# Performance work log

Measured on AMD Instinct MI355X. Metric: run time of the kernel, lower is better.

## Reference

```python
import jax, jax.numpy as jnp
import numpy as np

B, S, E, A = 64, 1024, 512, 128


def setup_inputs() -> dict:
    key = jax.random.key(0)
    ks = jax.random.split(key, 12)
    sc = 0.02
    states = jax.random.normal(ks[0], (B, S, E), jnp.float32)
    cls_token = jax.random.normal(ks[1], (B, E), jnp.float32)
    # ragged lengths in [2, S]; force at least one full-length row so padded width == S-1
    lengths = jax.random.randint(ks[2], (B,), 2, S + 1).at[0].set(S).astype(jnp.int32)
    position_action = (jax.random.randint(ks[3], (B,), 0, S) % (lengths - 1)).astype(jnp.int32)
    symbol_action = jax.random.randint(ks[4], (B,), 0, A).astype(jnp.int32)
    W1p = jax.random.normal(ks[5], (2 * E, 2 * E), jnp.float32) * sc
    b1p = jnp.zeros((2 * E,), jnp.float32)
    w2p = jax.random.normal(ks[6], (2 * E,), jnp.float32) * sc
    b2p = jnp.zeros((1,), jnp.float32)
    W1s = jax.random.normal(ks[7], (2 * E, 2 * E), jnp.float32) * sc
    b1s = jnp.zeros((2 * E,), jnp.float32)
    W2s = jax.random.normal(ks[8], (2 * E, A), jnp.float32) * sc
    b2s = jnp.zeros((A,), jnp.float32)
    Wc1 = jax.random.normal(ks[9], (E, E), jnp.float32) * sc
    bc1 = jnp.zeros((E,), jnp.float32)
    wc2 = jax.random.normal(ks[10], (E,), jnp.float32) * sc
    bc2 = jnp.zeros((1,), jnp.float32)
    return dict(states=states, cls_token=cls_token, W1p=W1p, b1p=b1p, w2p=w2p, b2p=b2p,
                W1s=W1s, b1s=b1s, W2s=W2s, b2s=b2s, Wc1=Wc1, bc1=bc1, wc2=wc2, bc2=bc2,
                lengths=lengths, position_action=position_action, symbol_action=symbol_action)


def reference(states, cls_token, W1p, b1p, w2p, b2p, W1s, b1s, W2s, b2s,
              Wc1, bc1, wc2, bc2, lengths, position_action, symbol_action):
    b, s, e = states.shape
    # --- get_adjacent_pairs + position_actor MLP, fused (no [.,2E] concat materialized) ---
    first, second = states[:, :-1], states[:, 1:]            # (B, S-1, E) each
    h = jax.nn.relu(jnp.einsum('bse,ef->bsf', first, W1p[:e])
                    + jnp.einsum('bse,ef->bsf', second, W1p[e:]) + b1p)  # (B, S-1, 2E)
    scores = jnp.einsum('bsf,f->bs', h, w2p) + b2p            # (B, S-1)
    # --- map_scores_to_sentences: pad invalid pair slots with -inf ---
    pos_mask = jnp.arange(s - 1)[None, :] < (lengths - 1)[:, None]
    scores = jnp.where(pos_mask, scores, -jnp.inf)
    logp = jax.nn.log_softmax(scores, axis=1)
    logp_pos = jnp.take_along_axis(logp, position_action[:, None], axis=1)[:, 0]
    logp_m = jnp.where(pos_mask, logp, 0.0)                   # safe for -inf slots
    ent_pos = -jnp.sum(jnp.exp(logp) * logp_m, axis=1)
    # --- symbol head on the pair embedding at the chosen split position ---
    bidx = jnp.arange(b)
    e1 = states[bidx, position_action]                        # (B, E)
    e2 = states[bidx, position_action + 1]                    # (B, E)
    sh = jax.nn.relu(e1 @ W1s[:e] + e2 @ W1s[e:] + b1s)       # (B, 2E)
    slogp = jax.nn.log_softmax(sh @ W2s + b2s, axis=1)        # (B, A)
    logp_sym = jnp.take_along_axis(slogp, symbol_action[:, None], axis=1)[:, 0]
    ent_sym = -jnp.sum(jnp.exp(slogp) * slogp, axis=1)
    # --- critic on cls token ---
    val = jax.nn.relu(cls_token @ Wc1 + bc1) @ wc2 + bc2      # (B,)
    return jnp.stack([logp_pos, logp_sym, val, ent_pos, ent_sym], axis=0)  # (5, B)
```

## Files before the change

### kernel.cpp

```cpp
#include <hip/hip_runtime.h>
#include <stdint.h>

#define BDIM 64
#define SDIM 1024
#define EDIM 512
#define ADIM 128
#define KDIM 1024
#define NDIM 1024

typedef unsigned short u16;
typedef __attribute__((ext_vector_type(8))) short short8;
typedef __attribute__((ext_vector_type(4))) float floatx4;
typedef const __attribute__((address_space(1))) void as1_void;
typedef __attribute__((address_space(3))) void as3_void;

__device__ inline u16 f2bf(float f){
  unsigned int u = __float_as_uint(f);
  u += 0x7fffu + ((u >> 16) & 1u);
  return (u16)(u >> 16);
}

__global__ __launch_bounds__(1024) void k_prep(
    const float* __restrict__ states,
    const float* __restrict__ W1p, const int* __restrict__ lengths,
    const int* __restrict__ pos_action,
    u16* __restrict__ sbf, u16* __restrict__ wt,
    int* __restrict__ rows, int* __restrict__ aux,
    float* __restrict__ scores)
{
  __shared__ float smem[64*65];
  const int blk = blockIdx.x, tid = threadIdx.x;

  if (blk < 1024){
    int i = blk*1024 + tid;
#pragma unroll
    for (int it = 0; it < 4; ++it, i += 1048576){
      int row = i >> 6;
      int s = row & 1023, b = row >> 10;
      if (s < lengths[b]){
        const float4* sp = (const float4*)states + (size_t)i*2;
        float4 a = sp[0], c = sp[1];
        short8 v;
        v[0]=(short)f2bf(a.x); v[1]=(short)f2bf(a.y); v[2]=(short)f2bf(a.z); v[3]=(short)f2bf(a.w);
        v[4]=(short)f2bf(c.x); v[5]=(short)f2bf(c.y); v[6]=(short)f2bf(c.z); v[7]=(short)f2bf(c.w);
        ((short8*)sbf)[i] = v;
      }
    }
    return;
  }
  if (blk < 1280){
    float (*tile)[65] = (float(*)[65])smem;
    int tb = blk - 1024;
    int zi = tb*1024 + tid;
    if (zi < 65536) scores[zi] = 0.f;
    int k0 = (tb & 15)*64, n0 = (tb >> 4)*64;
    int tx = tid & 63, ty = tid >> 6;
    for (int j = ty; j < 64; j += 16) tile[j][tx] = W1p[(size_t)(k0+j)*NDIM + n0 + tx];
    __syncthreads();
    for (int j = ty; j < 64; j += 16) wt[(size_t)(n0+j)*KDIM + k0 + tx] = f2bf(tile[tx][j]);
    return;
  }
  {
    __shared__ int scum[65];
    if (tid == 0){
      int c = 0;
      for (int b = 0; b < 64; ++b){ scum[b] = c; c += lengths[b] - 1; }
      scum[64] = c;
    }
    __syncthreads();
    if (tid < 65) aux[tid] = scum[tid];
    if (tid == 0){
      aux[70] = scum[64];
      aux[71] = (scum[64] + 127) >> 7;
    }
    if (tid < 64) rows[65472 + tid] = (tid << 10) + pos_action[tid];
    for (int b = 0; b < 64; ++b){
      int base = scum[b], L = scum[b+1] - scum[b];
      for (int i2 = tid; i2 < L; i2 += 1024) rows[base + i2] = (b << 10) + i2;
    }
  }
}

__global__ __launch_bounds__(256, 2) void k_gemm_scores(
    const u16* __restrict__ sbf, const u16* __restrict__ wt,
    const float* __restrict__ b1p, const float* __restrict__ w2p,
    const int* __restrict__ rows, const int* __restrict__ aux,
    float* __restrict__ scores,
    const float* __restrict__ cls,
    const float* __restrict__ W1s, const float* __restrict__ b1s,
    const float* __restrict__ Wc1, const float* __restrict__ bc1,
    const float* __restrict__ wc2, const float* __restrict__ bc2,
    float* __restrict__ sh, float* __restrict__ out)
{
  __shared__ short8 LDS[2048];
  const int tid = threadIdx.x;
  const int j = blockIdx.x;

  if (j < 8){
    short8* Ash = LDS;
    short8* Bsh = LDS + 512;
    const int w = tid >> 6, l = tid & 63;
    const int n0 = j * 128;
    const int lrow8 = l >> 3;
    const int c = (l & 7) ^ lrow8;
    const char* sbase = (const char*)sbf;
    int offA[2];
#pragma unroll
    for (int i = 0; i < 2; ++i){
      int mloc = (w*2 + i)*8 + lrow8;
      int rs = rows[65472 + mloc];
      offA[i] = rs*1024 + c*16;
    }
    const int r = l & 15, q = l >> 4;
    const int wm = w & 1, wn = w >> 1;
    int aIdx[2], bIdx[4];
#pragma unroll
    for (int i = 0; i < 2; ++i){
      int m = wm*32 + i*16 + r;
      aIdx[i] = m*8 + (q ^ (r & 7));
    }
#pragma unroll
    for (int i = 0; i < 4; ++i){
      int n = wn*64 + i*16 + r;
      bIdx[i] = n*8 + (q ^ (r & 7));
    }
    const int kt8 = tid >> 5, nq = tid & 31;
    floatx4 acc[2][4];
#pragma unroll
    for (int a = 0; a < 2; ++a)
#pragma unroll
      for (int b = 0; b < 4; ++b) acc[a][b] = (floatx4)(0.0f);

    for (int step = 0; step < 16; ++step){
      __syncthreads();
#pragma unroll
      for (int i = 0; i < 2; ++i)
        __builtin_amdgcn_global_load_lds((as1_void*)(sbase + offA[i] + step*128),
                                         (as3_void*)((char*)Ash + (w*2 + i)*1024), 16, 0, 0);
      const float* wsrc = W1s + (size_t)(step*64 + kt8*8)*1024 + n0 + nq*4;
      float v[8][4];
#pragma unroll
      for (int kk = 0; kk < 8; ++kk)
        *(float4*)v[kk] = *(const float4*)(wsrc + (size_t)kk*1024);
#pragma unroll
      for (int jj = 0; jj < 4; ++jj){
        short8 c8;
#pragma unroll
        for (int kk = 0; kk < 8; ++kk) c8[kk] = (short)f2bf(v[kk][jj]);
        int R = nq*4 + jj;
        Bsh[R*8 + (kt8 ^ (R & 7))] = c8;
      }
      __syncthreads();
#pragma unroll
      for (int kh = 0; kh < 2; ++kh){
        short8 af[2], bf[4];
#pragma unroll
        for (int i = 0; i < 2; ++i) af[i] = Ash[aIdx[i] ^ (kh*4)];
#pragma unroll
        for (int i = 0; i < 4; ++i) bf[i] = Bsh[bIdx[i] ^ (kh*4)];
#pragma unroll
        for (int mi = 0; mi < 2; ++mi)
#pragma unroll
          for (int ni = 0; ni < 4; ++ni)
            acc[mi][ni] = __builtin_amdgcn_mfma_f32_16x16x32_bf16(af[mi], bf[ni], acc[mi][ni], 0, 0, 0);
      }
    }
#pragma unroll
    for (int mi = 0; mi < 2; ++mi)
#pragma unroll
      for (int ni = 0; ni < 4; ++ni){
        int row = wm*32 + mi*16 + q*4;
        int col = n0 + wn*64 + ni*16 + r;
        floatx4 a = acc[mi][ni];
        float bb = b1s[col];
#pragma unroll
        for (int jj = 0; jj < 4; ++jj)
          sh[(row + jj)*1024 + col] = fmaxf(a[jj] + bb, 0.f);
      }
    return;
  }
  if (j < 72){
    float* xs = (float*)LDS;
    float* r2 = (float*)LDS + 512;
    int b = j - 8;
    xs[tid]       = cls[b*EDIM + tid];
    xs[tid + 256] = cls[b*EDIM + tid + 256];
    __syncthreads();
    float a0 = 0.f, a1 = 0.f;
#pragma unroll 8
    for (int k = 0; k < 512; ++k){
      float x = xs[k];
      a0 = fmaf(x, Wc1[(size_t)k*EDIM + tid],       a0);
      a1 = fmaf(x, Wc1[(size_t)k*EDIM + tid + 256], a1);
    }
    float p = fmaxf(a0 + bc1[tid],       0.f) * wc2[tid]
            + fmaxf(a1 + bc1[tid + 256], 0.f) * wc2[tid + 256];
    for (int off = 32; off; off >>= 1) p += __shfl_xor(p, off);
    if ((tid & 63) == 0) r2[tid >> 6] = p;
    __syncthreads();
    if (tid == 0) out[128 + b] = bc2[0] + r2[0] + r2[1] + r2[2] + r2[3];
    return;
  }

  short8* Ash = LDS;
  short8* Bsh = LDS + 1024;
  const int w = tid >> 6, l = tid & 63;
  const int jg = j - 72;
  const int tl = ((jg >> 6) << 3) | (jg & 7);
  const int nt = (jg >> 3) & 7;
  const int total = aux[70];
  if (tl >= aux[71]) return;

  const int lrow8 = l >> 3;
  const int c = (l & 7) ^ lrow8;
  const char* sbase = (const char*)sbf;
  const char* wbase = (const char*)wt;
  int offA[4], offB[4];
#pragma unroll
  for (int i = 0; i < 4; ++i){
    int mloc = (w*4 + i)*8 + lrow8;
    int mg = tl*128 + mloc;
    if (mg >= total) mg = 0;
    int rs = rows[mg];
    offA[i] = rs*1024 + c*16;
    int nloc = (w*4 + i)*8 + lrow8;
    offB[i] = (nt*128 + nloc)*2048 + c*16;
  }

  const int r = l & 15, q = l >> 4;
  const int wm = w & 1, wn = w >> 1;
  int aIdx[4], bIdx[4];
#pragma unroll
  for (int i = 0; i < 4; ++i){
    int m = wm*64 + i*16 + r;
    aIdx[i] = m*8 + (q ^ (r & 7));
    int n = wn*64 + i*16 + r;
    bIdx[i] = n*8 + (q ^ (r & 7));
  }

  floatx4 acc[4][4];
#pragma unroll
  for (int a = 0; a < 4; ++a)
#pragma unroll
    for (int b = 0; b < 4; ++b) acc[a][b] = (floatx4)(0.0f);

  for (int step = 0; step < 16; ++step){
    const int ktb = step * 128;
    __syncthreads();
#pragma unroll
    for (int i = 0; i < 4; ++i){
      __builtin_amdgcn_global_load_lds((as1_void*)(sbase + offA[i] + ktb),
                                       (as3_void*)((char*)Ash + (w*4 + i)*1024), 16, 0, 0);
    }
#pragma unroll
    for (int i = 0; i < 4; ++i){
      __builtin_amdgcn_global_load_lds((as1_void*)(wbase + offB[i] + ktb),
                                       (as3_void*)((char*)Bsh + (w*4 + i)*1024), 16, 0, 0);
    }
    __syncthreads();
#pragma unroll
    for (int kh = 0; kh < 2; ++kh){
      short8 af[4], bf[4];
#pragma unroll
      for (int i = 0; i < 4; ++i) af[i] = Ash[aIdx[i] ^ (kh*4)];
#pragma unroll
      for (int i = 0; i < 4; ++i) bf[i] = Bsh[bIdx[i] ^ (kh*4)];
#pragma unroll
      for (int mi = 0; mi < 4; ++mi)
#pragma unroll
        for (int ni = 0; ni < 4; ++ni)
          acc[mi][ni] = __builtin_amdgcn_mfma_f32_16x16x32_bf16(af[mi], bf[ni], acc[mi][ni], 0, 0, 0);
    }
  }

  const int mrow0 = tl*128 + wm*64;
  const int ncol0 = nt*128 + wn*64;
#pragma unroll
  for (int mi = 0; mi < 4; ++mi){
    float t0 = 0.f, t1 = 0.f, t2 = 0.f, t3 = 0.f;
#pragma unroll
    for (int ni = 0; ni < 4; ++ni){
      int n = ncol0 + ni*16 + r;
      float bb = b1p[n], ww = w2p[n];
      floatx4 a = acc[mi][ni];
      t0 += fmaxf(a[0] + bb, 0.f) * ww;
      t1 += fmaxf(a[1] + bb, 0.f) * ww;
      t2 += fmaxf(a[2] + bb, 0.f) * ww;
      t3 += fmaxf(a[3] + bb, 0.f) * ww;
    }
#pragma unroll
    for (int off = 1; off < 16; off <<= 1){
      t0 += __shfl_xor(t0, off);
      t1 += __shfl_xor(t1, off);
      t2 += __shfl_xor(t2, off);
      t3 += __shfl_xor(t3, off);
    }
    if (r == 0){
      int row = mrow0 + mi*16 + q*4;
      if (row + 0 < total) atomicAdd(&scores[row + 0], t0);
      if (row + 1 < total) atomicAdd(&scores[row + 1], t1);
      if (row + 2 < total) atomicAdd(&scores[row + 2], t2);
      if (row + 3 < total) atomicAdd(&scores[row + 3], t3);
    }
  }
}

__global__ __launch_bounds__(1024) void k_post(
    const float* __restrict__ scores, const float* __restrict__ sh,
    const float* __restrict__ W2s, const float* __restrict__ b2s,
    const int* __restrict__ aux, const int* __restrict__ lengths,
    const int* __restrict__ pos_action, const int* __restrict__ sym_action,
    float* __restrict__ out)
{
  __shared__ float smem[2208];
  const int blk = blockIdx.x, tid = threadIdx.x;
  if (blk < 64){
    float* sc   = smem;
    float* red  = smem + 1024;
    float* red2 = smem + 1040;
    int b = blk;
    int L = lengths[b] - 1;
    const float* sp = scores + aux[b];
    float mx = -1e30f;
    for (int s = tid; s < L; s += 1024){
      float v = sp[s];
      sc[s] = v;
      mx = fmaxf(mx, v);
    }
    for (int off = 32; off; off >>= 1) mx = fmaxf(mx, __shfl_xor(mx, off));
    if ((tid & 63) == 0) red[tid >> 6] = mx;
    __syncthreads();
    mx = -1e30f;
#pragma unroll
    for (int jj = 0; jj < 16; ++jj) mx = fmaxf(mx, red[jj]);
    float se = 0.f, ses = 0.f;
    for (int s = tid; s < L; s += 1024){
      float v = sc[s];
      float e = expf(v - mx);
      se += e; ses += e * v;
    }
    for (int off = 32; off; off >>= 1){ se += __shfl_xor(se, off); ses += __shfl_xor(ses, off); }
    __syncthreads();
    if ((tid & 63) == 0){ red[tid >> 6] = se; red2[tid >> 6] = ses; }
    __syncthreads();
    if (tid == 0){
      float S = 0.f, SS = 0.f;
#pragma unroll
      for (int jj = 0; jj < 16; ++jj){ S += red[jj]; SS += red2[jj]; }
      float logZ = logf(S);
      int pa = pos_action[b];
      out[b]       = sc[pa] - mx - logZ;
      out[192 + b] = mx + logZ - SS / S;
    }
    return;
  }
  {
    float* xs  = smem;
    float* red = smem + 1024;
    float* lg  = smem + 2048;
    float* r2  = smem + 2176;
    float* r3  = smem + 2192;
    int b = blk - 64;
    xs[tid] = sh[b*1024 + tid];
    __syncthreads();
    int n = tid & 127;
    int f0 = (tid >> 7) * 128;
    float acc = 0.f;
#pragma unroll 8
    for (int jj = 0; jj < 128; ++jj){
      int f = f0 + jj;
      acc = fmaf(xs[f], W2s[(size_t)f*ADIM + n], acc);
    }
    red[tid] = acc;
    __syncthreads();
    if (tid < 128){
      float s = b2s[tid];
#pragma unroll
      for (int jj = 0; jj < 8; ++jj) s += red[tid + jj*128];
      lg[tid] = s;
    }
    __syncthreads();
    float v = (tid < 128) ? lg[tid] : -1e30f;
    float mx = v;
    for (int off = 32; off; off >>= 1) mx = fmaxf(mx, __shfl_xor(mx, off));
    if ((tid & 63) == 0) r2[tid >> 6] = mx;
    __syncthreads();
    mx = -1e30f;
#pragma unroll
    for (int jj = 0; jj < 16; ++jj) mx = fmaxf(mx, r2[jj]);
    float e = (tid < 128) ? expf(v - mx) : 0.f;
    float se = e, ses = (tid < 128) ? e * v : 0.f;
    for (int off = 32; off; off >>= 1){ se += __shfl_xor(se, off); ses += __shfl_xor(ses, off); }
    __syncthreads();
    if ((tid & 63) == 0){ r2[tid >> 6] = se; r3[tid >> 6] = ses; }
    __syncthreads();
    if (tid == 0){
      float S = 0.f, SS = 0.f;
#pragma unroll
      for (int jj = 0; jj < 16; ++jj){ S += r2[jj]; SS += r3[jj]; }
      float logZ = logf(S);
      out[64 + b]  = lg[sym_action[b]] - mx - logZ;
      out[256 + b] = mx + logZ - SS / S;
    }
  }
}

extern "C" void kernel_launch(void* const* d_in, const int* in_sizes, int n_in,
                              void* d_out, int out_size, void* d_ws, size_t ws_size,
                              hipStream_t stream){
  const float* states = (const float*)d_in[0];
  const float* cls    = (const float*)d_in[1];
  const float* W1p    = (const float*)d_in[2];
  const float* b1p    = (const float*)d_in[3];
  const float* w2p    = (const float*)d_in[4];
  const float* W1s    = (const float*)d_in[6];
  const float* b1s    = (const float*)d_in[7];
  const float* W2s    = (const float*)d_in[8];
  const float* b2s    = (const float*)d_in[9];
  const float* Wc1    = (const float*)d_in[10];
  const float* bc1    = (const float*)d_in[11];
  const float* wc2    = (const float*)d_in[12];
  const float* bc2    = (const float*)d_in[13];
  const int* lengths  = (const int*)d_in[14];
  const int* pos_a    = (const int*)d_in[15];
  const int* sym_a    = (const int*)d_in[16];
  float* out = (float*)d_out;

  char* ws = (char*)d_ws;
  u16* sbf      = (u16*)ws;
  u16* wt       = (u16*)(ws + 67108864);
  float* scores = (float*)(ws + 69206016);
  float* sh     = (float*)(ws + 69468160);
  int* rows     = (int*)(ws + 69730304);
  int* aux      = (int*)(ws + 69992448);

  k_prep<<<1281, 1024, 0, stream>>>(states, W1p, lengths, pos_a, sbf, wt, rows, aux, scores);
  k_gemm_scores<<<4168, 256, 0, stream>>>(sbf, wt, b1p, w2p, rows, aux, scores,
                                          cls, W1s, b1s, Wc1, bc1, wc2, bc2, sh, out);
  k_post<<<128, 1024, 0, stream>>>(scores, sh, W2s, b2s, aux, lengths, pos_a, sym_a, out);
}
```

Before: 303.7 us.

## Run critic MLP as bf16 MFMA tiles and parallelize row-index build

The critic head, previously computed as 64 scalar-FMA blocks (one per batch row), becomes 4 MFMA blocks over 128-column slices of Wc1. A bf16 copy of the cls token is prepared in the prep kernel, and partial value dot products are reduced with atomics into an output preinitialized with bc2. The row-index/prefix-sum construction, formerly done by one serial block, is split across 64 blocks, one per batch. This trims launch size and serial prep work, but adds bf16 rounding to the critic and atomic, order-dependent summation.

```diff
diff --git a/kernel.cpp b/kernel.cpp
--- a/kernel.cpp
+++ b/kernel.cpp
@@ -21,12 +21,12 @@
 }
 
 __global__ __launch_bounds__(1024) void k_prep(
-    const float* __restrict__ states,
+    const float* __restrict__ states, const float* __restrict__ cls,
     const float* __restrict__ W1p, const int* __restrict__ lengths,
-    const int* __restrict__ pos_action,
-    u16* __restrict__ sbf, u16* __restrict__ wt,
+    const int* __restrict__ pos_action, const float* __restrict__ bc2,
+    u16* __restrict__ sbf, u16* __restrict__ wt, u16* __restrict__ clsbf,
     int* __restrict__ rows, int* __restrict__ aux,
-    float* __restrict__ scores)
+    float* __restrict__ scores, float* __restrict__ out)
 {
   __shared__ float smem[64*65];
   const int blk = blockIdx.x, tid = threadIdx.x;
@@ -60,23 +60,42 @@
     for (int j = ty; j < 64; j += 16) wt[(size_t)(n0+j)*KDIM + k0 + tx] = f2bf(tile[tx][j]);
     return;
   }
+  if (blk < 1344){
+    __shared__ int slen[64];
+    int bb = blk - 1280;
+    if (tid < 64) slen[tid] = lengths[tid];
+    __syncthreads();
+    int base = 0;
+    for (int b = 0; b < bb; ++b) base += slen[b] - 1;
+    int L = slen[bb] - 1;
+    if (tid < L) rows[base + tid] = (bb << 10) + tid;
+    if (bb == 0){
+      if (tid <= 64){
+        int c = 0;
+        for (int b = 0; b < tid; ++b) c += slen[b] - 1;
+        aux[tid] = c;
+        if (tid == 64){
+          aux[70] = c;
+          aux[71] = (c + 127) >> 7;
+        }
+      }
+      if (tid < 64){
+        rows[65472 + tid] = (tid << 10) + pos_action[tid];
+        out[128 + tid] = bc2[0];
+      }
+    }
+    return;
+  }
   {
-    __shared__ int scum[65];
-    if (tid == 0){
-      int c = 0;
-      for (int b = 0; b < 64; ++b){ scum[b] = c; c += lengths[b] - 1; }
-      scum[64] = c;
-    }
-    __syncthreads();
-    if (tid < 65) aux[tid] = scum[tid];
-    if (tid == 0){
-      aux[70] = scum[64];
-      aux[71] = (scum[64] + 127) >> 7;
-    }
-    if (tid < 64) rows[65472 + tid] = (tid << 10) + pos_action[tid];
-    for (int b = 0; b < 64; ++b){
-      int base = scum[b], L = scum[b+1] - scum[b];
-      for (int i2 = tid; i2 < L; i2 += 1024) rows[base + i2] = (b << 10) + i2;
+#pragma unroll
+    for (int it = 0; it < 4; ++it){
+      int idx = it*1024 + tid;
+      const float4* sp = (const float4*)cls + (size_t)idx*2;
+      float4 a = sp[0], c = sp[1];
+      short8 v;
+      v[0]=(short)f2bf(a.x); v[1]=(short)f2bf(a.y); v[2]=(short)f2bf(a.z); v[3]=(short)f2bf(a.w);
+      v[4]=(short)f2bf(c.x); v[5]=(short)f2bf(c.y); v[6]=(short)f2bf(c.z); v[7]=(short)f2bf(c.w);
+      ((short8*)clsbf)[idx] = v;
     }
   }
 }
@@ -86,10 +105,10 @@
     const float* __restrict__ b1p, const float* __restrict__ w2p,
     const int* __restrict__ rows, const int* __restrict__ aux,
     float* __restrict__ scores,
-    const float* __restrict__ cls,
+    const u16* __restrict__ clsbf,
     const float* __restrict__ W1s, const float* __restrict__ b1s,
     const float* __restrict__ Wc1, const float* __restrict__ bc1,
-    const float* __restrict__ wc2, const float* __restrict__ bc2,
+    const float* __restrict__ wc2,
     float* __restrict__ sh, float* __restrict__ out)
 {
   __shared__ short8 LDS[2048];
@@ -179,33 +198,109 @@
       }
     return;
   }
-  if (j < 72){
-    float* xs = (float*)LDS;
-    float* r2 = (float*)LDS + 512;
-    int b = j - 8;
-    xs[tid]       = cls[b*EDIM + tid];
-    xs[tid + 256] = cls[b*EDIM + tid + 256];
-    __syncthreads();
-    float a0 = 0.f, a1 = 0.f;
-#pragma unroll 8
-    for (int k = 0; k < 512; ++k){
-      float x = xs[k];
-      a0 = fmaf(x, Wc1[(size_t)k*EDIM + tid],       a0);
-      a1 = fmaf(x, Wc1[(size_t)k*EDIM + tid + 256], a1);
-    }
-    float p = fmaxf(a0 + bc1[tid],       0.f) * wc2[tid]
-            + fmaxf(a1 + bc1[tid + 256], 0.f) * wc2[tid + 256];
-    for (int off = 32; off; off >>= 1) p += __shfl_xor(p, off);
-    if ((tid & 63) == 0) r2[tid >> 6] = p;
-    __syncthreads();
-    if (tid == 0) out[128 + b] = bc2[0] + r2[0] + r2[1] + r2[2] + r2[3];
+  if (j < 12){
+    short8* Ash = LDS;
+    short8* Bsh = LDS + 512;
+    const int w = tid >> 6, l = tid & 63;
+    const int n0 = (j - 8) * 128;
+    const int lrow8 = l >> 3;
+    const int c = (l & 7) ^ lrow8;
+    const char* abase = (const char*)clsbf;
+    int offA[2];
+#pragma unroll
+    for (int i = 0; i < 2; ++i){
+      int mloc = (w*2 + i)*8 + lrow8;
+      offA[i] = mloc*1024 + c*16;
+    }
+    const int r = l & 15, q = l >> 4;
+    const int wm = w & 1, wn = w >> 1;
+    int aIdx[2], bIdx[4];
+#pragma unroll
+    for (int i = 0; i < 2; ++i){
+      int m = wm*32 + i*16 + r;
+      aIdx[i] = m*8 + (q ^ (r & 7));
+    }
+#pragma unroll
+    for (int i = 0; i < 4; ++i){
+      int n = wn*64 + i*16 + r;
+      bIdx[i] = n*8 + (q ^ (r & 7));
+    }
+    const int kt8 = tid >> 5, nq = tid & 31;
+    floatx4 acc[2][4];
+#pragma unroll
+    for (int a = 0; a < 2; ++a)
+#pragma unroll
+      for (int b = 0; b < 4; ++b) acc[a][b] = (floatx4)(0.0f);
+
+    for (int step = 0; step < 8; ++step){
+      __syncthreads();
+#pragma unroll
+      for (int i = 0; i < 2; ++i)
+        __builtin_amdgcn_global_load_lds((as1_void*)(abase + offA[i] + step*128),
+                                         (as3_void*)((char*)Ash + (w*2 + i)*1024), 16, 0, 0);
+      const float* wsrc = Wc1 + (size_t)(step*64 + kt8*8)*512 + n0 + nq*4;
+      float v[8][4];
+#pragma unroll
+      for (int kk = 0; kk < 8; ++kk)
+        *(float4*)v[kk] = *(const float4*)(wsrc + (size_t)kk*512);
+#pragma unroll
+      for (int jj = 0; jj < 4; ++jj){
+        short8 c8;
+#pragma unroll
+        for (int kk = 0; kk < 8; ++kk) c8[kk] = (short)f2bf(v[kk][jj]);
+        int R = nq*4 + jj;
+        Bsh[R*8 + (kt8 ^ (R & 7))] = c8;
+      }
+      __syncthreads();
+#pragma unroll
+      for (int kh = 0; kh < 2; ++kh){
+        short8 af[2], bf[4];
+#pragma unroll
+        for (int i = 0; i < 2; ++i) af[i] = Ash[aIdx[i] ^ (kh*4)];
+#pragma unroll
+        for (int i = 0; i < 4; ++i) bf[i] = Bsh[bIdx[i] ^ (kh*4)];
+#pragma unroll
+        for (int mi = 0; mi < 2; ++mi)
+#pragma unroll
+          for (int ni = 0; ni < 4; ++ni)
+            acc[mi][ni] = __builtin_amdgcn_mfma_f32_16x16x32_bf16(af[mi], bf[ni], acc[mi][ni], 0, 0, 0);
+      }
+    }
+#pragma unroll
+    for (int mi = 0; mi < 2; ++mi){
+      float p0 = 0.f, p1 = 0.f, p2 = 0.f, p3 = 0.f;
+#pragma unroll
+      for (int ni = 0; ni < 4; ++ni){
+        int col = n0 + wn*64 + ni*16 + r;
+        float bb = bc1[col], ww = wc2[col];
+        floatx4 a = acc[mi][ni];
+        p0 += fmaxf(a[0] + bb, 0.f) * ww;
+        p1 += fmaxf(a[1] + bb, 0.f) * ww;
+        p2 += fmaxf(a[2] + bb, 0.f) * ww;
+        p3 += fmaxf(a[3] + bb, 0.f) * ww;
+      }
+#pragma unroll
+      for (int off = 1; off < 16; off <<= 1){
+        p0 += __shfl_xor(p0, off);
+        p1 += __shfl_xor(p1, off);
+        p2 += __shfl_xor(p2, off);
+        p3 += __shfl_xor(p3, off);
+      }
+      if (r == 0){
+        int row = wm*32 + mi*16 + q*4;
+        atomicAdd(&out[128 + row + 0], p0);
+        atomicAdd(&out[128 + row + 1], p1);
+        atomicAdd(&out[128 + row + 2], p2);
+        atomicAdd(&out[128 + row + 3], p3);
+      }
+    }
     return;
   }
 
   short8* Ash = LDS;
   short8* Bsh = LDS + 1024;
   const int w = tid >> 6, l = tid & 63;
-  const int jg = j - 72;
+  const int jg = j - 12;
   const int tl = ((jg >> 6) << 3) | (jg & 7);
   const int nt = (jg >> 3) & 7;
   const int total = aux[70];
@@ -433,9 +528,11 @@
   float* sh     = (float*)(ws + 69468160);
   int* rows     = (int*)(ws + 69730304);
   int* aux      = (int*)(ws + 69992448);
-
-  k_prep<<<1281, 1024, 0, stream>>>(states, W1p, lengths, pos_a, sbf, wt, rows, aux, scores);
-  k_gemm_scores<<<4168, 256, 0, stream>>>(sbf, wt, b1p, w2p, rows, aux, scores,
-                                          cls, W1s, b1s, Wc1, bc1, wc2, bc2, sh, out);
+  u16* clsbf    = (u16*)(ws + 70000640);
+
+  k_prep<<<1345, 1024, 0, stream>>>(states, cls, W1p, lengths, pos_a, bc2,
+                                    sbf, wt, clsbf, rows, aux, scores, out);
+  k_gemm_scores<<<4108, 256, 0, stream>>>(sbf, wt, b1p, w2p, rows, aux, scores,
+                                          clsbf, W1s, b1s, Wc1, bc1, wc2, sh, out);
   k_post<<<128, 1024, 0, stream>>>(scores, sh, W2s, b2s, aux, lengths, pos_a, sym_a, out);
 }
```

Measured after the change: 308.5 us. No clear change (+1.6%).
